# Optimization experiments

Measured on AMD Instinct MI355X. Metric: run time of the kernel, lower is better.

Reference implementation:

```python
import jax, jax.numpy as jnp
import numpy as np

NEG_INF = jnp.float32(-1e30)  # stand-in for -inf; relu(-inf) == relu(-1e30) == 0


def setup_inputs() -> dict:
    key = jax.random.key(0)
    ks = jax.random.split(key, 8)
    B, S, E = 4, 4096, 512
    query = jax.random.normal(ks[0], (B, S, E), dtype=jnp.float32)
    k_in = jax.random.normal(ks[1], (B, S, E), dtype=jnp.float32)
    v_in = jax.random.normal(ks[2], (B, S, E), dtype=jnp.float32)
    mask = jax.random.randint(ks[3], (B, S, S), 0, 2) > 0  # bool [B,S,S]
    scale = 1.0 / np.sqrt(E)
    W1 = jax.random.uniform(ks[4], (E, E), jnp.float32, -scale, scale)
    b1 = jax.random.uniform(ks[5], (E,), jnp.float32, -scale, scale)
    W2 = jax.random.uniform(ks[6], (E, E), jnp.float32, -scale, scale)
    b2 = jax.random.uniform(ks[7], (E,), jnp.float32, -scale, scale)
    return {"query": query, "key": k_in, "value": v_in, "mask": mask,
            "W1": W1, "b1": b1, "W2": W2, "b2": b2}


def reference(query, key, value, mask, W1, b1, W2, b2):
    # key projection: nn.Linear -> x @ W.T + b
    k = jnp.einsum('bse,fe->bsf', key, W1) + b1
    # raw dot-product correlation scores [B, S, S]
    scores = jnp.einsum('bqe,bke->bqk', query, k)
    # module forces mask[:, :, 0] = True, then fills ~mask with -inf
    m = mask.at[:, :, 0].set(True)
    scores = jnp.where(m, scores, NEG_INF)
    # ReLU instead of softmax (no normalization); dropout is identity in eval
    alpha = jax.nn.relu(scores)
    # value projection then AV matmul
    v = jnp.einsum('bse,fe->bsf', value, W2) + b2
    out = jnp.einsum('bqk,bke->bqe', alpha, v)
    return out
```

## Files before the change

kernel.cpp:

```cpp
#include <hip/hip_runtime.h>
#include <cstdint>


typedef __bf16 bf16x8 __attribute__((ext_vector_type(8)));
typedef float f32x4 __attribute__((ext_vector_type(4)));

__device__ __forceinline__ unsigned short f2bf(float f) {
  unsigned int u = __float_as_uint(f);
  u += 0x7fffu + ((u >> 16) & 1u);
  return (unsigned short)(u >> 16);
}

__device__ __forceinline__ void async_load16(const void* g, void* l) {
  __builtin_amdgcn_global_load_lds(
      (const __attribute__((address_space(1))) unsigned int*)(uintptr_t)g,
      (__attribute__((address_space(3))) unsigned int*)(unsigned int)(uintptr_t)l,
      16, 0, 0);
}

__global__ void __launch_bounds__(256)
prep(const float* __restrict__ q, const float* __restrict__ k,
     const float* __restrict__ v, const float* __restrict__ w1,
     const float* __restrict__ w2, const int* __restrict__ m,
     unsigned short* __restrict__ qb, unsigned short* __restrict__ kb,
     unsigned short* __restrict__ vb, unsigned short* __restrict__ w1b,
     unsigned short* __restrict__ w2b, unsigned int* __restrict__ bits) {
  const int b = blockIdx.x, tid = threadIdx.x;
  if (b < 24576) {
    const int which = b >> 13;
    const int idx = (b & 8191) * 256 + tid;
    const float* in = (which == 0) ? q : (which == 1) ? k : v;
    unsigned short* out = (which == 0) ? qb : (which == 1) ? kb : vb;
    float4 f = ((const float4*)in)[idx];
    ushort4 o;
    o.x = f2bf(f.x); o.y = f2bf(f.y); o.z = f2bf(f.z); o.w = f2bf(f.w);
    ((ushort4*)out)[idx] = o;
  } else if (b < 25088) {
    const int which = (b - 24576) >> 8;
    const int idx = ((b - 24576) & 255) * 256 + tid;
    const float* in = (which == 0) ? w1 : w2;
    unsigned short* out = (which == 0) ? w1b : w2b;
    float4 f = ((const float4*)in)[idx];
    ushort4 o;
    o.x = f2bf(f.x); o.y = f2bf(f.y); o.z = f2bf(f.z); o.w = f2bf(f.w);
    ((ushort4*)out)[idx] = o;
  } else {
    const int lane = tid & 63;
    const size_t wid = (size_t)(b - 25088) * 4 + (tid >> 6);
    const size_t base = wid * 256;
    unsigned long long bl[4];
#pragma unroll
    for (int c = 0; c < 4; ++c) {
      size_t e = base + (size_t)c * 64 + lane;
      int col = (int)(e & 4095);
      bl[c] = __ballot((m[e] != 0) || (col == 0));
    }
    if (lane < 8)
      bits[base / 32 + lane] = (unsigned int)(bl[lane >> 1] >> ((lane & 1) * 32));
  }
}

__global__ void __launch_bounds__(256)
proj(const unsigned short* __restrict__ Kb, const unsigned short* __restrict__ W1b,
     unsigned short* __restrict__ Kp, const float* __restrict__ b1,
     const unsigned short* __restrict__ W2b, const unsigned short* __restrict__ Vb,
     unsigned short* __restrict__ Vpt, const float* __restrict__ b2) {
  constexpr int K = 512;
  constexpr long long SE = 4096LL * 512;
  __shared__ unsigned short sA[2 * 128 * 32];
  __shared__ unsigned short sB[2 * 128 * 32];

  const int L = blockIdx.x;
  const unsigned short *Ab, *Bb;
  unsigned short* C;
  const float* bias;
  int tm0, tn0, N, epi;
  if (L < 512) {
    tn0 = (L & 3) * 128; tm0 = (L >> 2) * 128;
    Ab = Kb; Bb = W1b; C = Kp; bias = b1; N = 512; epi = 0;
  } else {
    const int t = L - 512;
    tn0 = (t & 31) * 128; tm0 = ((t >> 5) & 3) * 128;
    const int bz = t >> 7;
    Ab = W2b; Bb = Vb + (size_t)bz * SE; C = Vpt + (size_t)bz * SE;
    bias = b2; N = 4096; epi = 1;
  }

  const int tid = threadIdx.x;
  const int lane = tid & 63, wave = tid >> 6;
  const int ldrow = lane >> 2, lcol = (lane & 3) * 8;
  const int wm = (wave >> 1) * 64, wn = (wave & 1) * 64;
  const int lr = lane & 15, lq = lane >> 4;

  f32x4 acc[4][4] = {};

  for (int k0 = 0; k0 < K; k0 += 64) {
#pragma unroll
    for (int g = 0; g < 2; ++g)
#pragma unroll
      for (int l = 0; l < 2; ++l) {
        const int row = wave * 32 + l * 16;
        async_load16(Ab + (size_t)(tm0 + row + ldrow) * K + (k0 + g * 32 + lcol),
                     &sA[g * 4096 + row * 32]);
        async_load16(Bb + (size_t)(tn0 + row + ldrow) * K + (k0 + g * 32 + lcol),
                     &sB[g * 4096 + row * 32]);
      }
    __syncthreads();
#pragma unroll
    for (int g = 0; g < 2; ++g) {
      bf16x8 af[4], bfr[4];
#pragma unroll
      for (int t = 0; t < 4; ++t) {
        af[t]  = *(const bf16x8*)&sA[g * 4096 + (wm + t * 16 + lr) * 32 + lq * 8];
        bfr[t] = *(const bf16x8*)&sB[g * 4096 + (wn + t * 16 + lr) * 32 + lq * 8];
      }
#pragma unroll
      for (int mt = 0; mt < 4; ++mt)
#pragma unroll
        for (int nt = 0; nt < 4; ++nt)
          acc[mt][nt] = __builtin_amdgcn_mfma_f32_16x16x32_bf16(af[mt], bfr[nt],
                                                                acc[mt][nt], 0, 0, 0);
    }
    __syncthreads();
  }

#pragma unroll
  for (int mt = 0; mt < 4; ++mt)
#pragma unroll
    for (int r = 0; r < 4; ++r) {
      const int mm = tm0 + wm + mt * 16 + lq * 4 + r;
#pragma unroll
      for (int nt = 0; nt < 4; ++nt) {
        const int n = tn0 + wn + nt * 16 + lr;
        float v = acc[mt][nt][r];
        v += (epi == 0) ? bias[n] : bias[mm];
        C[(size_t)mm * N + n] = f2bf(v);
      }
    }
}

template <int EPI>
__global__ void __launch_bounds__(512, 2)
gemm256(const unsigned short* __restrict__ A, const unsigned short* __restrict__ B,
        void* __restrict__ Cout, const unsigned int* __restrict__ mbits,
        int M, int N, int K,
        long long strA, long long strB, long long strC, long long strM) {
  __shared__ unsigned short sA[2][256][64];
  __shared__ unsigned short sB[2][256][64];

  int lin = blockIdx.x;
  lin = (lin & 7) * ((int)gridDim.x >> 3) + (lin >> 3);
  const int tilesN = N >> 8;
  const int tilesM = M >> 8;
  const int bx = lin % tilesN;
  const int by = (lin / tilesN) % tilesM;
  const int bz = lin / (tilesN * tilesM);

  const int tn0 = bx << 8, tm0 = by << 8;
  const unsigned short* Ab = A + (size_t)bz * strA;
  const unsigned short* Bb = B + (size_t)bz * strB;

  const int tid  = threadIdx.x;
  const int lane = tid & 63;
  const int w    = tid >> 6;
  const int wr   = w >> 2;
  const int wc   = w & 3;
  const int lr   = lane & 15;
  const int lq   = lane >> 4;

  const int srow = tid >> 3;
  const int scol = (((tid & 7) ^ (srow & 7)) << 3);
  const int sdst = tid << 4;

#define STAGE64(bufbase, g, t0, k0, R0)                                      \
  async_load16((g) + (size_t)((t0) + (R0) + srow) * K + (k0) + scol,         \
               (char*)(bufbase) + ((R0) << 7) + sdst)

  const int sxor  = (lr & 7) << 4;
  const int k0off = (lq << 4) ^ sxor;
  const int k1off = (64 | (lq << 4)) ^ sxor;
  const int aRow  = (wr * 128 + lr) * 128;
  const int bRow  = (wc * 64 + lr) * 128;

#define LDA(d, mh, mt2, kk)                                                  \
  (*(const bf16x8*)((const char*)sA[d] + aRow + (mh) * 8192 + (mt2) * 2048 + \
                    k##kk##off))
#define LDB(d, nh, nt2, kk)                                                  \
  (*(const bf16x8*)((const char*)sB[d] + bRow + (nh) * 4096 + (nt2) * 2048 + \
                    k##kk##off))

  f32x4 acc[8][4] = {};
  bf16x8 afr[4][2];
  bf16x8 bfr[4][2];

#define RDA(d, mh)                                                           \
  _Pragma("unroll") for (int mt2 = 0; mt2 < 4; ++mt2) {                      \
    afr[mt2][0] = LDA(d, mh, mt2, 0);                                        \
    afr[mt2][1] = LDA(d, mh, mt2, 1);                                        \
  }
#define RDB(d, nh)                                                           \
  _Pragma("unroll") for (int nt2 = 0; nt2 < 2; ++nt2) {                      \
    bfr[(nh) * 2 + nt2][0] = LDB(d, nh, nt2, 0);                             \
    bfr[(nh) * 2 + nt2][1] = LDB(d, nh, nt2, 1);                             \
  }
#define MFMAQ(mh, nh)                                                        \
  __builtin_amdgcn_s_setprio(1);                                             \
  _Pragma("unroll") for (int mt2 = 0; mt2 < 4; ++mt2)                        \
  _Pragma("unroll") for (int nt2 = 0; nt2 < 2; ++nt2) {                      \
    acc[(mh) * 4 + mt2][(nh) * 2 + nt2] =                                    \
        __builtin_amdgcn_mfma_f32_16x16x32_bf16(                             \
            afr[mt2][0], bfr[(nh) * 2 + nt2][0],                             \
            acc[(mh) * 4 + mt2][(nh) * 2 + nt2], 0, 0, 0);                   \
    acc[(mh) * 4 + mt2][(nh) * 2 + nt2] =                                    \
        __builtin_amdgcn_mfma_f32_16x16x32_bf16(                             \
            afr[mt2][1], bfr[(nh) * 2 + nt2][1],                             \
            acc[(mh) * 4 + mt2][(nh) * 2 + nt2], 0, 0, 0);                   \
  }                                                                          \
  __builtin_amdgcn_s_setprio(0);
#define BAR __builtin_amdgcn_s_barrier()

  const int nIter = K >> 7;

  STAGE64(sB[0], Bb, tn0, 0, 0);   STAGE64(sB[0], Bb, tn0, 0, 64);
  STAGE64(sB[0], Bb, tn0, 0, 128); STAGE64(sB[0], Bb, tn0, 0, 192);
  STAGE64(sA[0], Ab, tm0, 0, 0);   STAGE64(sA[0], Ab, tm0, 0, 64);
  STAGE64(sA[0], Ab, tm0, 0, 128); STAGE64(sA[0], Ab, tm0, 0, 192);
  STAGE64(sB[1], Bb, tn0, 64, 0);  STAGE64(sB[1], Bb, tn0, 64, 64);
  STAGE64(sB[1], Bb, tn0, 64, 128);STAGE64(sB[1], Bb, tn0, 64, 192);
  asm volatile("s_waitcnt vmcnt(4)" ::: "memory");
  BAR;

  for (int j = 0; j < nIter; ++j) {
    const int kb = j << 7;
    const bool pf = (j + 1 < nIter);
    RDA(0, 0); RDB(0, 0);
    STAGE64(sA[1], Ab, tm0, kb + 64, 0);
    STAGE64(sA[1], Ab, tm0, kb + 64, 64);
    BAR; MFMAQ(0, 0); BAR;
    RDB(0, 1);
    STAGE64(sA[1], Ab, tm0, kb + 64, 128);
    STAGE64(sA[1], Ab, tm0, kb + 64, 192);
    BAR; MFMAQ(0, 1); BAR;
    RDA(0, 1);
    if (pf) { STAGE64(sB[0], Bb, tn0, kb + 128, 0);
              STAGE64(sB[0], Bb, tn0, kb + 128, 64); }
    BAR; MFMAQ(1, 1); BAR;
    if (pf) { STAGE64(sB[0], Bb, tn0, kb + 128, 128);
              STAGE64(sB[0], Bb, tn0, kb + 128, 192); }
    BAR; MFMAQ(1, 0);
    if (pf) asm volatile("s_waitcnt vmcnt(4)" ::: "memory");
    else    asm volatile("s_waitcnt vmcnt(0)" ::: "memory");
    BAR;
    RDA(1, 0); RDB(1, 0);
    if (pf) { STAGE64(sA[0], Ab, tm0, kb + 128, 0);
              STAGE64(sA[0], Ab, tm0, kb + 128, 64); }
    BAR; MFMAQ(0, 0); BAR;
    RDB(1, 1);
    if (pf) { STAGE64(sA[0], Ab, tm0, kb + 128, 128);
              STAGE64(sA[0], Ab, tm0, kb + 128, 192); }
    BAR; MFMAQ(0, 1); BAR;
    RDA(1, 1);
    if (pf) { STAGE64(sB[1], Bb, tn0, kb + 192, 0);
              STAGE64(sB[1], Bb, tn0, kb + 192, 64); }
    BAR; MFMAQ(1, 1); BAR;
    if (pf) { STAGE64(sB[1], Bb, tn0, kb + 192, 128);
              STAGE64(sB[1], Bb, tn0, kb + 192, 192); }
    BAR; MFMAQ(1, 0);
    asm volatile("s_waitcnt vmcnt(4)" ::: "memory");
    BAR;
  }

#pragma unroll
  for (int mt = 0; mt < 8; ++mt) {
#pragma unroll
    for (int r = 0; r < 4; ++r) {
      const int m = tm0 + wr * 128 + mt * 16 + lq * 4 + r;
      unsigned long long w64 = 0;
      if constexpr (EPI == 2) {
        w64 = *(const unsigned long long*)&mbits[(size_t)bz * strM +
                                                 (size_t)m * (N >> 5) +
                                                 ((tn0 + wc * 64) >> 5)];
      }
#pragma unroll
      for (int nt = 0; nt < 4; ++nt) {
        const int n = tn0 + wc * 64 + nt * 16 + lr;
        float v = acc[mt][nt][r];
        if constexpr (EPI == 2) {
          v = ((w64 >> (nt * 16 + lr)) & 1ull) ? fmaxf(v, 0.f) : 0.f;
          ((unsigned short*)Cout)[(size_t)bz * strC + (size_t)m * N + n] = f2bf(v);
        } else {
          ((float*)Cout)[(size_t)bz * strC + (size_t)m * N + n] = v;
        }
      }
    }
  }
#undef STAGE64
#undef LDA
#undef LDB
#undef RDA
#undef RDB
#undef MFMAQ
#undef BAR
}

__global__ void __launch_bounds__(512, 2)
outgemm(const unsigned short* __restrict__ A, const unsigned short* __restrict__ B,
        float* __restrict__ Cout, int M, int N, int K,
        long long strA, long long strB, long long strC) {
  __shared__ unsigned short sA[2][256][64];
  __shared__ unsigned short sB[2][128][64];

  int lin = blockIdx.x;
  lin = (lin & 7) * ((int)gridDim.x >> 3) + (lin >> 3);
  const int tilesN = N >> 7;
  const int tilesM = M >> 8;
  const int bx = lin % tilesN;
  const int by = (lin / tilesN) % tilesM;
  const int bz = lin / (tilesN * tilesM);

  const int tn0 = bx << 7, tm0 = by << 8;
  const unsigned short* Ab = A + (size_t)bz * strA;
  const unsigned short* Bb = B + (size_t)bz * strB;

  const int tid  = threadIdx.x;
  const int lane = tid & 63;
  const int w    = tid >> 6;
  const int wr   = w >> 2;
  const int wc   = w & 3;
  const int lr   = lane & 15;
  const int lq   = lane >> 4;

  const int srow = tid >> 3;
  const int scol = (((tid & 7) ^ (srow & 7)) << 3);
  const int sdst = tid << 4;

#define OST(bufbase, g, t0, k0, R0)                                          \
  async_load16((g) + (size_t)((t0) + (R0) + srow) * K + (k0) + scol,         \
               (char*)(bufbase) + ((R0) << 7) + sdst)

  const int sxor  = (lr & 7) << 4;
  const int k0off = (lq << 4) ^ sxor;
  const int k1off = (64 | (lq << 4)) ^ sxor;
  const int aRow  = (wr * 128 + lr) * 128;
  const int bRow  = (wc * 32 + lr) * 128;

#define OLDA(d, mh, mt2, kk)                                                 \
  (*(const bf16x8*)((const char*)sA[d] + aRow + (mh) * 8192 + (mt2) * 2048 + \
                    k##kk##off))
#define OLDB(d, nt, kk)                                                      \
  (*(const bf16x8*)((const char*)sB[d] + bRow + (nt) * 2048 + k##kk##off))

  f32x4 acc[8][2] = {};
  bf16x8 afr[4][2];
  bf16x8 bfr[2][2];

#define ORDA(d, mh)                                                          \
  _Pragma("unroll") for (int mt2 = 0; mt2 < 4; ++mt2) {                      \
    afr[mt2][0] = OLDA(d, mh, mt2, 0);                                       \
    afr[mt2][1] = OLDA(d, mh, mt2, 1);                                       \
  }
#define ORDB(d, nt)                                                          \
  { bfr[nt][0] = OLDB(d, nt, 0); bfr[nt][1] = OLDB(d, nt, 1); }
#define OMFMAQ(mh, nt)                                                       \
  __builtin_amdgcn_s_setprio(1);                                             \
  _Pragma("unroll") for (int mt2 = 0; mt2 < 4; ++mt2) {                      \
    acc[(mh) * 4 + mt2][nt] = __builtin_amdgcn_mfma_f32_16x16x32_bf16(       \
        afr[mt2][0], bfr[nt][0], acc[(mh) * 4 + mt2][nt], 0, 0, 0);          \
    acc[(mh) * 4 + mt2][nt] = __builtin_amdgcn_mfma_f32_16x16x32_bf16(       \
        afr[mt2][1], bfr[nt][1], acc[(mh) * 4 + mt2][nt], 0, 0, 0);          \
  }                                                                          \
  __builtin_amdgcn_s_setprio(0);
#define OBAR __builtin_amdgcn_s_barrier()

  const int nIter = K >> 7;

  OST(sB[0], Bb, tn0, 0, 0);   OST(sB[0], Bb, tn0, 0, 64);
  OST(sA[0], Ab, tm0, 0, 0);   OST(sA[0], Ab, tm0, 0, 64);
  OST(sA[0], Ab, tm0, 0, 128); OST(sA[0], Ab, tm0, 0, 192);
  OST(sB[1], Bb, tn0, 64, 0);  OST(sB[1], Bb, tn0, 64, 64);
  asm volatile("s_waitcnt vmcnt(2)" ::: "memory");
  OBAR;

  for (int j = 0; j < nIter; ++j) {
    const int kb = j << 7;
    const bool pf = (j + 1 < nIter);
    ORDA(0, 0); ORDB(0, 0);
    OST(sA[1], Ab, tm0, kb + 64, 0);
    OST(sA[1], Ab, tm0, kb + 64, 64);
    OBAR; OMFMAQ(0, 0); OBAR;
    ORDB(0, 1);
    OST(sA[1], Ab, tm0, kb + 64, 128);
    OST(sA[1], Ab, tm0, kb + 64, 192);
    OBAR; OMFMAQ(0, 1); OBAR;
    ORDA(0, 1);
    if (pf) OST(sB[0], Bb, tn0, kb + 128, 0);
    OBAR; OMFMAQ(1, 1); OBAR;
    if (pf) OST(sB[0], Bb, tn0, kb + 128, 64);
    OBAR; OMFMAQ(1, 0);
    if (pf) asm volatile("s_waitcnt vmcnt(2)" ::: "memory");
    else    asm volatile("s_waitcnt vmcnt(0)" ::: "memory");
    OBAR;
    ORDA(1, 0); ORDB(1, 0);
    if (pf) { OST(sA[0], Ab, tm0, kb + 128, 0);
              OST(sA[0], Ab, tm0, kb + 128, 64); }
    OBAR; OMFMAQ(0, 0); OBAR;
    ORDB(1, 1);
    if (pf) { OST(sA[0], Ab, tm0, kb + 128, 128);
              OST(sA[0], Ab, tm0, kb + 128, 192); }
    OBAR; OMFMAQ(0, 1); OBAR;
    ORDA(1, 1);
    if (pf) OST(sB[1], Bb, tn0, kb + 192, 0);
    OBAR; OMFMAQ(1, 1); OBAR;
    if (pf) OST(sB[1], Bb, tn0, kb + 192, 64);
    OBAR; OMFMAQ(1, 0);
    asm volatile("s_waitcnt vmcnt(2)" ::: "memory");
    OBAR;
  }

#pragma unroll
  for (int mt = 0; mt < 8; ++mt) {
#pragma unroll
    for (int r = 0; r < 4; ++r) {
      const int m = tm0 + wr * 128 + mt * 16 + lq * 4 + r;
#pragma unroll
      for (int nt = 0; nt < 2; ++nt) {
        const int n = tn0 + wc * 32 + nt * 16 + lr;
        Cout[(size_t)bz * strC + (size_t)m * N + n] = acc[mt][nt][r];
      }
    }
  }
#undef OST
#undef OLDA
#undef OLDB
#undef ORDA
#undef ORDB
#undef OMFMAQ
#undef OBAR
}

extern "C" void kernel_launch(void* const* d_in, const int* in_sizes, int n_in,
                              void* d_out, int out_size, void* d_ws, size_t ws_size,
                              hipStream_t stream) {
  const float* query = (const float*)d_in[0];
  const float* key   = (const float*)d_in[1];
  const float* value = (const float*)d_in[2];
  const int*   mask  = (const int*)d_in[3];
  const float* W1    = (const float*)d_in[4];
  const float* b1    = (const float*)d_in[5];
  const float* W2    = (const float*)d_in[6];
  const float* b2    = (const float*)d_in[7];
  float* out = (float*)d_out;

  constexpr int B = 4, S = 4096, E = 512;
  constexpr long long BSE = (long long)B * S * E;
  constexpr long long SE  = (long long)S * E;
  constexpr long long SS  = (long long)S * S;
  constexpr long long BSS = (long long)B * S * S;
  constexpr long long EE  = (long long)E * E;

  char* ws = (char*)d_ws;
  unsigned short* Qb   = (unsigned short*)ws;  ws += BSE * 2;
  unsigned short* Kb   = (unsigned short*)ws;  ws += BSE * 2;
  unsigned short* Vb   = (unsigned short*)ws;  ws += BSE * 2;
  unsigned short* W1b  = (unsigned short*)ws;  ws += EE * 2;
  unsigned short* W2b  = (unsigned short*)ws;  ws += EE * 2;
  unsigned short* Kp   = (unsigned short*)ws;  ws += BSE * 2;
  unsigned short* Vpt  = (unsigned short*)ws;  ws += BSE * 2;
  unsigned short* alph = (unsigned short*)ws;  ws += BSS * 2;
  unsigned int*   mbit = (unsigned int*)ws;    ws += BSS / 8;

  prep<<<dim3(24576 + 512 + 65536), 256, 0, stream>>>(
      query, key, value, W1, W2, mask, Qb, Kb, Vb, W1b, W2b, mbit);

  proj<<<dim3(1024), 256, 0, stream>>>(Kb, W1b, Kp, b1, W2b, Vb, Vpt, b2);

  gemm256<2><<<dim3((S / 256) * (S / 256) * B), 512, 0, stream>>>(
      Qb, Kp, alph, mbit, S, S, E, SE, SE, SS, SS / 32);

  outgemm<<<dim3((E / 128) * (S / 256) * B), 512, 0, stream>>>(
      alph, Vpt, out, S, E, S, SS, SE, SE);
}
```

Measured before the change: 631.0 us.

## Make alpha GEMM persistent across batches and merge outgemm MFMA phases

The alpha score GEMM now launches one block per (m,n) tile and loops over all four batches. The K-stage pipeline runs continuously across batch boundaries, and the masked-ReLU epilogue is written every 8 K-steps before the accumulators are reset. The intent is to cut the pipeline prologue and drain per tile and keep the loads flowing across batches, at the cost of a grid four times smaller (256 blocks), which may underfill the CUs. The output GEMM also merges its MFMA quarter-phases into halves with fewer barriers, and its loads are batched together.

Result: slower. 691.9 us (+9.6%).

```diff
diff --git a/kernel.cpp b/kernel.cpp
--- a/kernel.cpp
+++ b/kernel.cpp
@@ -139,26 +139,20 @@
     }
 }
 
-template <int EPI>
 __global__ void __launch_bounds__(512, 2)
-gemm256(const unsigned short* __restrict__ A, const unsigned short* __restrict__ B,
-        void* __restrict__ Cout, const unsigned int* __restrict__ mbits,
-        int M, int N, int K,
-        long long strA, long long strB, long long strC, long long strM) {
+alpha256(const unsigned short* __restrict__ A, const unsigned short* __restrict__ B,
+         unsigned short* __restrict__ Cw, const unsigned int* __restrict__ mbits,
+         int M, int N, int K,
+         long long strA, long long strB, long long strC, long long strM) {
   __shared__ unsigned short sA[2][256][64];
   __shared__ unsigned short sB[2][256][64];
 
   int lin = blockIdx.x;
   lin = (lin & 7) * ((int)gridDim.x >> 3) + (lin >> 3);
-  const int tilesN = N >> 8;
-  const int tilesM = M >> 8;
-  const int bx = lin % tilesN;
-  const int by = (lin / tilesN) % tilesM;
-  const int bz = lin / (tilesN * tilesM);
+  const int bx = lin & 15;
+  const int by = lin >> 4;
 
   const int tn0 = bx << 8, tm0 = by << 8;
-  const unsigned short* Ab = A + (size_t)bz * strA;
-  const unsigned short* Bb = B + (size_t)bz * strB;
 
   const int tid  = threadIdx.x;
   const int lane = tid & 63;
@@ -172,9 +166,20 @@
   const int scol = (((tid & 7) ^ (srow & 7)) << 3);
   const int sdst = tid << 4;
 
-#define STAGE64(bufbase, g, t0, k0, R0)                                      \
-  async_load16((g) + (size_t)((t0) + (R0) + srow) * K + (k0) + scol,         \
-               (char*)(bufbase) + ((R0) << 7) + sdst)
+#define STG_A(bufbase, gk, R0)                                               \
+  if ((gk) < 32) {                                                           \
+    const unsigned short* P_ = A + (size_t)((gk) >> 3) * strA;               \
+    async_load16(P_ + (size_t)(tm0 + (R0) + srow) * K + (((gk) & 7) << 6) +  \
+                     scol,                                                   \
+                 (char*)(bufbase) + ((R0) << 7) + sdst);                     \
+  }
+#define STG_B(bufbase, gk, R0)                                               \
+  if ((gk) < 32) {                                                           \
+    const unsigned short* P_ = B + (size_t)((gk) >> 3) * strB;               \
+    async_load16(P_ + (size_t)(tn0 + (R0) + srow) * K + (((gk) & 7) << 6) +  \
+                     scol,                                                   \
+                 (char*)(bufbase) + ((R0) << 7) + sdst);                     \
+  }
 
   const int sxor  = (lr & 7) << 4;
   const int k0off = (lq << 4) ^ sxor;
@@ -219,82 +224,74 @@
   __builtin_amdgcn_s_setprio(0);
 #define BAR __builtin_amdgcn_s_barrier()
 
-  const int nIter = K >> 7;
-
-  STAGE64(sB[0], Bb, tn0, 0, 0);   STAGE64(sB[0], Bb, tn0, 0, 64);
-  STAGE64(sB[0], Bb, tn0, 0, 128); STAGE64(sB[0], Bb, tn0, 0, 192);
-  STAGE64(sA[0], Ab, tm0, 0, 0);   STAGE64(sA[0], Ab, tm0, 0, 64);
-  STAGE64(sA[0], Ab, tm0, 0, 128); STAGE64(sA[0], Ab, tm0, 0, 192);
-  STAGE64(sB[1], Bb, tn0, 64, 0);  STAGE64(sB[1], Bb, tn0, 64, 64);
-  STAGE64(sB[1], Bb, tn0, 64, 128);STAGE64(sB[1], Bb, tn0, 64, 192);
+  STG_B(sB[0], 0, 0);   STG_B(sB[0], 0, 64);
+  STG_B(sB[0], 0, 128); STG_B(sB[0], 0, 192);
+  STG_A(sA[0], 0, 0);   STG_A(sA[0], 0, 64);
+  STG_A(sA[0], 0, 128); STG_A(sA[0], 0, 192);
+  STG_B(sB[1], 1, 0);   STG_B(sB[1], 1, 64);
+  STG_B(sB[1], 1, 128); STG_B(sB[1], 1, 192);
   asm volatile("s_waitcnt vmcnt(4)" ::: "memory");
   BAR;
 
-  for (int j = 0; j < nIter; ++j) {
-    const int kb = j << 7;
-    const bool pf = (j + 1 < nIter);
+  for (int s = 0; s < 16; ++s) {
+    const int gk0 = 2 * s, gk1 = gk0 + 1;
     RDA(0, 0); RDB(0, 0);
-    STAGE64(sA[1], Ab, tm0, kb + 64, 0);
-    STAGE64(sA[1], Ab, tm0, kb + 64, 64);
+    STG_A(sA[1], gk1, 0); STG_A(sA[1], gk1, 64);
     BAR; MFMAQ(0, 0); BAR;
     RDB(0, 1);
-    STAGE64(sA[1], Ab, tm0, kb + 64, 128);
-    STAGE64(sA[1], Ab, tm0, kb + 64, 192);
+    STG_A(sA[1], gk1, 128); STG_A(sA[1], gk1, 192);
     BAR; MFMAQ(0, 1); BAR;
     RDA(0, 1);
-    if (pf) { STAGE64(sB[0], Bb, tn0, kb + 128, 0);
-              STAGE64(sB[0], Bb, tn0, kb + 128, 64); }
+    STG_B(sB[0], gk0 + 2, 0); STG_B(sB[0], gk0 + 2, 64);
     BAR; MFMAQ(1, 1); BAR;
-    if (pf) { STAGE64(sB[0], Bb, tn0, kb + 128, 128);
-              STAGE64(sB[0], Bb, tn0, kb + 128, 192); }
+    STG_B(sB[0], gk0 + 2, 128); STG_B(sB[0], gk0 + 2, 192);
     BAR; MFMAQ(1, 0);
-    if (pf) asm volatile("s_waitcnt vmcnt(4)" ::: "memory");
-    else    asm volatile("s_waitcnt vmcnt(0)" ::: "memory");
+    if (gk0 + 2 < 32) asm volatile("s_waitcnt vmcnt(4)" ::: "memory");
+    else              asm volatile("s_waitcnt vmcnt(0)" ::: "memory");
     BAR;
     RDA(1, 0); RDB(1, 0);
-    if (pf) { STAGE64(sA[0], Ab, tm0, kb + 128, 0);
-              STAGE64(sA[0], Ab, tm0, kb + 128, 64); }
+    STG_A(sA[0], gk0 + 2, 0); STG_A(sA[0], gk0 + 2, 64);
     BAR; MFMAQ(0, 0); BAR;
     RDB(1, 1);
-    if (pf) { STAGE64(sA[0], Ab, tm0, kb + 128, 128);
-              STAGE64(sA[0], Ab, tm0, kb + 128, 192); }
+    STG_A(sA[0], gk0 + 2, 128); STG_A(sA[0], gk0 + 2, 192);
     BAR; MFMAQ(0, 1); BAR;
     RDA(1, 1);
-    if (pf) { STAGE64(sB[1], Bb, tn0, kb + 192, 0);
-              STAGE64(sB[1], Bb, tn0, kb + 192, 64); }
+    STG_B(sB[1], gk0 + 3, 0); STG_B(sB[1], gk0 + 3, 64);
     BAR; MFMAQ(1, 1); BAR;
-    if (pf) { STAGE64(sB[1], Bb, tn0, kb + 192, 128);
-              STAGE64(sB[1], Bb, tn0, kb + 192, 192); }
+    STG_B(sB[1], gk0 + 3, 128); STG_B(sB[1], gk0 + 3, 192);
     BAR; MFMAQ(1, 0);
     asm volatile("s_waitcnt vmcnt(4)" ::: "memory");
     BAR;
-  }
-
-#pragma unroll
-  for (int mt = 0; mt < 8; ++mt) {
-#pragma unroll
-    for (int r = 0; r < 4; ++r) {
-      const int m = tm0 + wr * 128 + mt * 16 + lq * 4 + r;
-      unsigned long long w64 = 0;
-      if constexpr (EPI == 2) {
-        w64 = *(const unsigned long long*)&mbits[(size_t)bz * strM +
+
+    if ((s & 3) == 3) {
+      const int tz = s >> 2;
+#pragma unroll
+      for (int mt = 0; mt < 8; ++mt) {
+#pragma unroll
+        for (int r = 0; r < 4; ++r) {
+          const int m = tm0 + wr * 128 + mt * 16 + lq * 4 + r;
+          unsigned long long w64 =
+              *(const unsigned long long*)&mbits[(size_t)tz * strM +
                                                  (size_t)m * (N >> 5) +
                                                  ((tn0 + wc * 64) >> 5)];
-      }
-#pragma unroll
-      for (int nt = 0; nt < 4; ++nt) {
-        const int n = tn0 + wc * 64 + nt * 16 + lr;
-        float v = acc[mt][nt][r];
-        if constexpr (EPI == 2) {
-          v = ((w64 >> (nt * 16 + lr)) & 1ull) ? fmaxf(v, 0.f) : 0.f;
-          ((unsigned short*)Cout)[(size_t)bz * strC + (size_t)m * N + n] = f2bf(v);
-        } else {
-          ((float*)Cout)[(size_t)bz * strC + (size_t)m * N + n] = v;
+#pragma unroll
+          for (int nt = 0; nt < 4; ++nt) {
+            const int n = tn0 + wc * 64 + nt * 16 + lr;
+            float v = acc[mt][nt][r];
+            v = ((w64 >> (nt * 16 + lr)) & 1ull) ? fmaxf(v, 0.f) : 0.f;
+            Cw[(size_t)tz * strC + (size_t)m * N + n] = f2bf(v);
+          }
         }
       }
+      const f32x4 z = {0.f, 0.f, 0.f, 0.f};
+#pragma unroll
+      for (int mt = 0; mt < 8; ++mt)
+#pragma unroll
+        for (int nt = 0; nt < 4; ++nt) acc[mt][nt] = z;
     }
   }
-#undef STAGE64
+#undef STG_A
+#undef STG_B
 #undef LDA
 #undef LDB
 #undef RDA
@@ -359,11 +356,13 @@
     afr[mt2][0] = OLDA(d, mh, mt2, 0);                                       \
     afr[mt2][1] = OLDA(d, mh, mt2, 1);                                       \
   }
-#define ORDB(d, nt)                                                          \
-  { bfr[nt][0] = OLDB(d, nt, 0); bfr[nt][1] = OLDB(d, nt, 1); }
-#define OMFMAQ(mh, nt)                                                       \
+#define ORDBB(d)                                                             \
+  { bfr[0][0] = OLDB(d, 0, 0); bfr[0][1] = OLDB(d, 0, 1);                    \
+    bfr[1][0] = OLDB(d, 1, 0); bfr[1][1] = OLDB(d, 1, 1); }
+#define OMFMA16(mh)                                                          \
   __builtin_amdgcn_s_setprio(1);                                             \
-  _Pragma("unroll") for (int mt2 = 0; mt2 < 4; ++mt2) {                      \
+  _Pragma("unroll") for (int mt2 = 0; mt2 < 4; ++mt2)                        \
+  _Pragma("unroll") for (int nt = 0; nt < 2; ++nt) {                         \
     acc[(mh) * 4 + mt2][nt] = __builtin_amdgcn_mfma_f32_16x16x32_bf16(       \
         afr[mt2][0], bfr[nt][0], acc[(mh) * 4 + mt2][nt], 0, 0, 0);          \
     acc[(mh) * 4 + mt2][nt] = __builtin_amdgcn_mfma_f32_16x16x32_bf16(       \
@@ -384,36 +383,29 @@
   for (int j = 0; j < nIter; ++j) {
     const int kb = j << 7;
     const bool pf = (j + 1 < nIter);
-    ORDA(0, 0); ORDB(0, 0);
-    OST(sA[1], Ab, tm0, kb + 64, 0);
-    OST(sA[1], Ab, tm0, kb + 64, 64);
-    OBAR; OMFMAQ(0, 0); OBAR;
-    ORDB(0, 1);
-    OST(sA[1], Ab, tm0, kb + 64, 128);
-    OST(sA[1], Ab, tm0, kb + 64, 192);
-    OBAR; OMFMAQ(0, 1); OBAR;
+    ORDA(0, 0); ORDBB(0);
+    OST(sA[1], Ab, tm0, kb + 64, 0);   OST(sA[1], Ab, tm0, kb + 64, 64);
+    OST(sA[1], Ab, tm0, kb + 64, 128); OST(sA[1], Ab, tm0, kb + 64, 192);
+    OBAR; OMFMA16(0); OBAR;
     ORDA(0, 1);
-    if (pf) OST(sB[0], Bb, tn0, kb + 128, 0);
-    OBAR; OMFMAQ(1, 1); OBAR;
-    if (pf) OST(sB[0], Bb, tn0, kb + 128, 64);
-    OBAR; OMFMAQ(1, 0);
+    if (pf) { OST(sB[0], Bb, tn0, kb + 128, 0);
+              OST(sB[0], Bb, tn0, kb + 128, 64); }
+    OBAR; OMFMA16(1);
     if (pf) asm volatile("s_waitcnt vmcnt(2)" ::: "memory");
     else    asm volatile("s_waitcnt vmcnt(0)" ::: "memory");
     OBAR;
-    ORDA(1, 0); ORDB(1, 0);
+    ORDA(1, 0); ORDBB(1);
     if (pf) { OST(sA[0], Ab, tm0, kb + 128, 0);
-              OST(sA[0], Ab, tm0, kb + 128, 64); }
-    OBAR; OMFMAQ(0, 0); OBAR;
-    ORDB(1, 1);
-    if (pf) { OST(sA[0], Ab, tm0, kb + 128, 128);
+              OST(sA[0], Ab, tm0, kb + 128, 64);
+              OST(sA[0], Ab, tm0, kb + 128, 128);
               OST(sA[0], Ab, tm0, kb + 128, 192); }
-    OBAR; OMFMAQ(0, 1); OBAR;
+    OBAR; OMFMA16(0); OBAR;
     ORDA(1, 1);
-    if (pf) OST(sB[1], Bb, tn0, kb + 192, 0);
-    OBAR; OMFMAQ(1, 1); OBAR;
-    if (pf) OST(sB[1], Bb, tn0, kb + 192, 64);
-    OBAR; OMFMAQ(1, 0);
-    asm volatile("s_waitcnt vmcnt(2)" ::: "memory");
+    if (pf) { OST(sB[1], Bb, tn0, kb + 192, 0);
+              OST(sB[1], Bb, tn0, kb + 192, 64); }
+    OBAR; OMFMA16(1);
+    if (pf) asm volatile("s_waitcnt vmcnt(2)" ::: "memory");
+    else    asm volatile("s_waitcnt vmcnt(0)" ::: "memory");
     OBAR;
   }
 
@@ -433,8 +425,8 @@
 #undef OLDA
 #undef OLDB
 #undef ORDA
-#undef ORDB
-#undef OMFMAQ
+#undef ORDBB
+#undef OMFMA16
 #undef OBAR
 }
 
@@ -474,7 +466,7 @@
 
   proj<<<dim3(1024), 256, 0, stream>>>(Kb, W1b, Kp, b1, W2b, Vb, Vpt, b2);
 
-  gemm256<2><<<dim3((S / 256) * (S / 256) * B), 512, 0, stream>>>(
+  alpha256<<<dim3((S / 256) * (S / 256)), 512, 0, stream>>>(
       Qb, Kp, alph, mbit, S, S, E, SE, SE, SS, SS / 32);
 
   outgemm<<<dim3((E / 128) * (S / 256) * B), 512, 0, stream>>>(
```

## Make alpha GEMM persistent over batch and retile output GEMM to 128x256

Applied to the files above, without the earlier changes.

The scores/alpha kernel now launches 256 blocks, one per 256x256 tile, and each block loops over the 4 batches, dropping the per-batch grid dimension and the template epilogue switch. The output GEMM swaps its tile shape from 256x128 to 128x256 (M by N), loading more of the V operand per block and less of alpha, with adjusted staging and wait counts. The intent is to cut launch or tail imbalance and improve operand reuse. The risk is that only 256 blocks may underfill the GPU and serialize the batch work inside each block.

Result: slower. 725.2 us (+14.9%).

```diff
diff --git a/kernel.cpp b/kernel.cpp
--- a/kernel.cpp
+++ b/kernel.cpp
@@ -139,26 +139,19 @@
     }
 }
 
-template <int EPI>
 __global__ void __launch_bounds__(512, 2)
-gemm256(const unsigned short* __restrict__ A, const unsigned short* __restrict__ B,
-        void* __restrict__ Cout, const unsigned int* __restrict__ mbits,
-        int M, int N, int K,
-        long long strA, long long strB, long long strC, long long strM) {
+alpha256p(const unsigned short* __restrict__ A, const unsigned short* __restrict__ B,
+          unsigned short* __restrict__ Cw, const unsigned int* __restrict__ mbits,
+          int M, int N, int K,
+          long long strA, long long strB, long long strC, long long strM) {
   __shared__ unsigned short sA[2][256][64];
   __shared__ unsigned short sB[2][256][64];
 
   int lin = blockIdx.x;
-  lin = (lin & 7) * ((int)gridDim.x >> 3) + (lin >> 3);
-  const int tilesN = N >> 8;
-  const int tilesM = M >> 8;
-  const int bx = lin % tilesN;
-  const int by = (lin / tilesN) % tilesM;
-  const int bz = lin / (tilesN * tilesM);
-
+  lin = (lin & 7) * 32 + (lin >> 3);
+  const int bx = lin & 15;
+  const int by = lin >> 4;
   const int tn0 = bx << 8, tm0 = by << 8;
-  const unsigned short* Ab = A + (size_t)bz * strA;
-  const unsigned short* Bb = B + (size_t)bz * strB;
 
   const int tid  = threadIdx.x;
   const int lane = tid & 63;
@@ -189,7 +182,6 @@
   (*(const bf16x8*)((const char*)sB[d] + bRow + (nh) * 4096 + (nt2) * 2048 + \
                     k##kk##off))
 
-  f32x4 acc[8][4] = {};
   bf16x8 afr[4][2];
   bf16x8 bfr[4][2];
 
@@ -221,75 +213,76 @@
 
   const int nIter = K >> 7;
 
-  STAGE64(sB[0], Bb, tn0, 0, 0);   STAGE64(sB[0], Bb, tn0, 0, 64);
-  STAGE64(sB[0], Bb, tn0, 0, 128); STAGE64(sB[0], Bb, tn0, 0, 192);
-  STAGE64(sA[0], Ab, tm0, 0, 0);   STAGE64(sA[0], Ab, tm0, 0, 64);
-  STAGE64(sA[0], Ab, tm0, 0, 128); STAGE64(sA[0], Ab, tm0, 0, 192);
-  STAGE64(sB[1], Bb, tn0, 64, 0);  STAGE64(sB[1], Bb, tn0, 64, 64);
-  STAGE64(sB[1], Bb, tn0, 64, 128);STAGE64(sB[1], Bb, tn0, 64, 192);
-  asm volatile("s_waitcnt vmcnt(4)" ::: "memory");
-  BAR;
-
-  for (int j = 0; j < nIter; ++j) {
-    const int kb = j << 7;
-    const bool pf = (j + 1 < nIter);
-    RDA(0, 0); RDB(0, 0);
-    STAGE64(sA[1], Ab, tm0, kb + 64, 0);
-    STAGE64(sA[1], Ab, tm0, kb + 64, 64);
-    BAR; MFMAQ(0, 0); BAR;
-    RDB(0, 1);
-    STAGE64(sA[1], Ab, tm0, kb + 64, 128);
-    STAGE64(sA[1], Ab, tm0, kb + 64, 192);
-    BAR; MFMAQ(0, 1); BAR;
-    RDA(0, 1);
-    if (pf) { STAGE64(sB[0], Bb, tn0, kb + 128, 0);
-              STAGE64(sB[0], Bb, tn0, kb + 128, 64); }
-    BAR; MFMAQ(1, 1); BAR;
-    if (pf) { STAGE64(sB[0], Bb, tn0, kb + 128, 128);
-              STAGE64(sB[0], Bb, tn0, kb + 128, 192); }
-    BAR; MFMAQ(1, 0);
-    if (pf) asm volatile("s_waitcnt vmcnt(4)" ::: "memory");
-    else    asm volatile("s_waitcnt vmcnt(0)" ::: "memory");
-    BAR;
-    RDA(1, 0); RDB(1, 0);
-    if (pf) { STAGE64(sA[0], Ab, tm0, kb + 128, 0);
-              STAGE64(sA[0], Ab, tm0, kb + 128, 64); }
-    BAR; MFMAQ(0, 0); BAR;
-    RDB(1, 1);
-    if (pf) { STAGE64(sA[0], Ab, tm0, kb + 128, 128);
-              STAGE64(sA[0], Ab, tm0, kb + 128, 192); }
-    BAR; MFMAQ(0, 1); BAR;
-    RDA(1, 1);
-    if (pf) { STAGE64(sB[1], Bb, tn0, kb + 192, 0);
-              STAGE64(sB[1], Bb, tn0, kb + 192, 64); }
-    BAR; MFMAQ(1, 1); BAR;
-    if (pf) { STAGE64(sB[1], Bb, tn0, kb + 192, 128);
-              STAGE64(sB[1], Bb, tn0, kb + 192, 192); }
-    BAR; MFMAQ(1, 0);
+  for (int vz = 0; vz < 4; ++vz) {
+    const unsigned short* Ab = A + (size_t)vz * strA;
+    const unsigned short* Bb = B + (size_t)vz * strB;
+
+    f32x4 acc[8][4] = {};
+
+    STAGE64(sB[0], Bb, tn0, 0, 0);   STAGE64(sB[0], Bb, tn0, 0, 64);
+    STAGE64(sB[0], Bb, tn0, 0, 128); STAGE64(sB[0], Bb, tn0, 0, 192);
+    STAGE64(sA[0], Ab, tm0, 0, 0);   STAGE64(sA[0], Ab, tm0, 0, 64);
+    STAGE64(sA[0], Ab, tm0, 0, 128); STAGE64(sA[0], Ab, tm0, 0, 192);
+    STAGE64(sB[1], Bb, tn0, 64, 0);  STAGE64(sB[1], Bb, tn0, 64, 64);
+    STAGE64(sB[1], Bb, tn0, 64, 128);STAGE64(sB[1], Bb, tn0, 64, 192);
     asm volatile("s_waitcnt vmcnt(4)" ::: "memory");
     BAR;
-  }
-
-#pragma unroll
-  for (int mt = 0; mt < 8; ++mt) {
-#pragma unroll
-    for (int r = 0; r < 4; ++r) {
-      const int m = tm0 + wr * 128 + mt * 16 + lq * 4 + r;
-      unsigned long long w64 = 0;
-      if constexpr (EPI == 2) {
-        w64 = *(const unsigned long long*)&mbits[(size_t)bz * strM +
-                                                 (size_t)m * (N >> 5) +
-                                                 ((tn0 + wc * 64) >> 5)];
-      }
-#pragma unroll
-      for (int nt = 0; nt < 4; ++nt) {
-        const int n = tn0 + wc * 64 + nt * 16 + lr;
-        float v = acc[mt][nt][r];
-        if constexpr (EPI == 2) {
+
+    for (int j = 0; j < nIter; ++j) {
+      const int kb = j << 7;
+      const bool pf = (j + 1 < nIter);
+      RDA(0, 0); RDB(0, 0);
+      STAGE64(sA[1], Ab, tm0, kb + 64, 0);
+      STAGE64(sA[1], Ab, tm0, kb + 64, 64);
+      BAR; MFMAQ(0, 0); BAR;
+      RDB(0, 1);
+      STAGE64(sA[1], Ab, tm0, kb + 64, 128);
+      STAGE64(sA[1], Ab, tm0, kb + 64, 192);
+      BAR; MFMAQ(0, 1); BAR;
+      RDA(0, 1);
+      if (pf) { STAGE64(sB[0], Bb, tn0, kb + 128, 0);
+                STAGE64(sB[0], Bb, tn0, kb + 128, 64); }
+      BAR; MFMAQ(1, 1); BAR;
+      if (pf) { STAGE64(sB[0], Bb, tn0, kb + 128, 128);
+                STAGE64(sB[0], Bb, tn0, kb + 128, 192); }
+      BAR; MFMAQ(1, 0);
+      if (pf) asm volatile("s_waitcnt vmcnt(4)" ::: "memory");
+      else    asm volatile("s_waitcnt vmcnt(0)" ::: "memory");
+      BAR;
+      RDA(1, 0); RDB(1, 0);
+      if (pf) { STAGE64(sA[0], Ab, tm0, kb + 128, 0);
+                STAGE64(sA[0], Ab, tm0, kb + 128, 64); }
+      BAR; MFMAQ(0, 0); BAR;
+      RDB(1, 1);
+      if (pf) { STAGE64(sA[0], Ab, tm0, kb + 128, 128);
+                STAGE64(sA[0], Ab, tm0, kb + 128, 192); }
+      BAR; MFMAQ(0, 1); BAR;
+      RDA(1, 1);
+      if (pf) { STAGE64(sB[1], Bb, tn0, kb + 192, 0);
+                STAGE64(sB[1], Bb, tn0, kb + 192, 64); }
+      BAR; MFMAQ(1, 1); BAR;
+      if (pf) { STAGE64(sB[1], Bb, tn0, kb + 192, 128);
+                STAGE64(sB[1], Bb, tn0, kb + 192, 192); }
+      BAR; MFMAQ(1, 0);
+      asm volatile("s_waitcnt vmcnt(4)" ::: "memory");
+      BAR;
+    }
+
+#pragma unroll
+    for (int mt = 0; mt < 8; ++mt) {
+#pragma unroll
+      for (int r = 0; r < 4; ++r) {
+        const int m = tm0 + wr * 128 + mt * 16 + lq * 4 + r;
+        unsigned long long w64 =
+            *(const unsigned long long*)&mbits[(size_t)vz * strM +
+                                               (size_t)m * (N >> 5) +
+                                               ((tn0 + wc * 64) >> 5)];
+#pragma unroll
+        for (int nt = 0; nt < 4; ++nt) {
+          const int n = tn0 + wc * 64 + nt * 16 + lr;
+          float v = acc[mt][nt][r];
           v = ((w64 >> (nt * 16 + lr)) & 1ull) ? fmaxf(v, 0.f) : 0.f;
-          ((unsigned short*)Cout)[(size_t)bz * strC + (size_t)m * N + n] = f2bf(v);
-        } else {
-          ((float*)Cout)[(size_t)bz * strC + (size_t)m * N + n] = v;
+          Cw[(size_t)vz * strC + (size_t)m * N + n] = f2bf(v);
         }
       }
     }
@@ -304,21 +297,21 @@
 }
 
 __global__ void __launch_bounds__(512, 2)
-outgemm(const unsigned short* __restrict__ A, const unsigned short* __restrict__ B,
-        float* __restrict__ Cout, int M, int N, int K,
-        long long strA, long long strB, long long strC) {
-  __shared__ unsigned short sA[2][256][64];
-  __shared__ unsigned short sB[2][128][64];
+outg(const unsigned short* __restrict__ A, const unsigned short* __restrict__ B,
+     float* __restrict__ Cout, int M, int N, int K,
+     long long strA, long long strB, long long strC) {
+  __shared__ unsigned short sA[2][128][64];
+  __shared__ unsigned short sB[2][256][64];
 
   int lin = blockIdx.x;
   lin = (lin & 7) * ((int)gridDim.x >> 3) + (lin >> 3);
-  const int tilesN = N >> 7;
-  const int tilesM = M >> 8;
+  const int tilesN = N >> 8;
+  const int tilesM = M >> 7;
   const int bx = lin % tilesN;
   const int by = (lin / tilesN) % tilesM;
   const int bz = lin / (tilesN * tilesM);
 
-  const int tn0 = bx << 7, tm0 = by << 8;
+  const int tn0 = bx << 8, tm0 = by << 7;
   const unsigned short* Ab = A + (size_t)bz * strA;
   const unsigned short* Bb = B + (size_t)bz * strB;
 
@@ -341,33 +334,42 @@
   const int sxor  = (lr & 7) << 4;
   const int k0off = (lq << 4) ^ sxor;
   const int k1off = (64 | (lq << 4)) ^ sxor;
-  const int aRow  = (wr * 128 + lr) * 128;
-  const int bRow  = (wc * 32 + lr) * 128;
+  const int aRow  = (wr * 64 + lr) * 128;
+  const int bRow  = (wc * 64 + lr) * 128;
 
 #define OLDA(d, mh, mt2, kk)                                                 \
-  (*(const bf16x8*)((const char*)sA[d] + aRow + (mh) * 8192 + (mt2) * 2048 + \
+  (*(const bf16x8*)((const char*)sA[d] + aRow + (mh) * 4096 + (mt2) * 2048 + \
                     k##kk##off))
-#define OLDB(d, nt, kk)                                                      \
-  (*(const bf16x8*)((const char*)sB[d] + bRow + (nt) * 2048 + k##kk##off))
-
-  f32x4 acc[8][2] = {};
-  bf16x8 afr[4][2];
-  bf16x8 bfr[2][2];
+#define OLDB(d, nh, nt2, kk)                                                 \
+  (*(const bf16x8*)((const char*)sB[d] + bRow + (nh) * 4096 + (nt2) * 2048 + \
+                    k##kk##off))
+
+  f32x4 acc[4][4] = {};
+  bf16x8 afr[2][2];
+  bf16x8 bfr[4][2];
 
 #define ORDA(d, mh)                                                          \
-  _Pragma("unroll") for (int mt2 = 0; mt2 < 4; ++mt2) {                      \
+  _Pragma("unroll") for (int mt2 = 0; mt2 < 2; ++mt2) {                      \
     afr[mt2][0] = OLDA(d, mh, mt2, 0);                                       \
     afr[mt2][1] = OLDA(d, mh, mt2, 1);                                       \
   }
-#define ORDB(d, nt)                                                          \
-  { bfr[nt][0] = OLDB(d, nt, 0); bfr[nt][1] = OLDB(d, nt, 1); }
-#define OMFMAQ(mh, nt)                                                       \
+#define ORDB(d, nh)                                                          \
+  _Pragma("unroll") for (int nt2 = 0; nt2 < 2; ++nt2) {                      \
+    bfr[(nh) * 2 + nt2][0] = OLDB(d, nh, nt2, 0);                            \
+    bfr[(nh) * 2 + nt2][1] = OLDB(d, nh, nt2, 1);                            \
+  }
+#define OMFMAQ(mh, nh)                                                       \
   __builtin_amdgcn_s_setprio(1);                                             \
-  _Pragma("unroll") for (int mt2 = 0; mt2 < 4; ++mt2) {                      \
-    acc[(mh) * 4 + mt2][nt] = __builtin_amdgcn_mfma_f32_16x16x32_bf16(       \
-        afr[mt2][0], bfr[nt][0], acc[(mh) * 4 + mt2][nt], 0, 0, 0);          \
-    acc[(mh) * 4 + mt2][nt] = __builtin_amdgcn_mfma_f32_16x16x32_bf16(       \
-        afr[mt2][1], bfr[nt][1], acc[(mh) * 4 + mt2][nt], 0, 0, 0);          \
+  _Pragma("unroll") for (int mt2 = 0; mt2 < 2; ++mt2)                        \
+  _Pragma("unroll") for (int nt2 = 0; nt2 < 2; ++nt2) {                      \
+    acc[(mh) * 2 + mt2][(nh) * 2 + nt2] =                                    \
+        __builtin_amdgcn_mfma_f32_16x16x32_bf16(                             \
+            afr[mt2][0], bfr[(nh) * 2 + nt2][0],                             \
+            acc[(mh) * 2 + mt2][(nh) * 2 + nt2], 0, 0, 0);                   \
+    acc[(mh) * 2 + mt2][(nh) * 2 + nt2] =                                    \
+        __builtin_amdgcn_mfma_f32_16x16x32_bf16(                             \
+            afr[mt2][1], bfr[(nh) * 2 + nt2][1],                             \
+            acc[(mh) * 2 + mt2][(nh) * 2 + nt2], 0, 0, 0);                   \
   }                                                                          \
   __builtin_amdgcn_s_setprio(0);
 #define OBAR __builtin_amdgcn_s_barrier()
@@ -375,10 +377,11 @@
   const int nIter = K >> 7;
 
   OST(sB[0], Bb, tn0, 0, 0);   OST(sB[0], Bb, tn0, 0, 64);
+  OST(sB[0], Bb, tn0, 0, 128); OST(sB[0], Bb, tn0, 0, 192);
   OST(sA[0], Ab, tm0, 0, 0);   OST(sA[0], Ab, tm0, 0, 64);
-  OST(sA[0], Ab, tm0, 0, 128); OST(sA[0], Ab, tm0, 0, 192);
   OST(sB[1], Bb, tn0, 64, 0);  OST(sB[1], Bb, tn0, 64, 64);
-  asm volatile("s_waitcnt vmcnt(2)" ::: "memory");
+  OST(sB[1], Bb, tn0, 64, 128);OST(sB[1], Bb, tn0, 64, 192);
+  asm volatile("s_waitcnt vmcnt(4)" ::: "memory");
   OBAR;
 
   for (int j = 0; j < nIter; ++j) {
@@ -389,15 +392,15 @@
     OST(sA[1], Ab, tm0, kb + 64, 64);
     OBAR; OMFMAQ(0, 0); OBAR;
     ORDB(0, 1);
-    OST(sA[1], Ab, tm0, kb + 64, 128);
-    OST(sA[1], Ab, tm0, kb + 64, 192);
     OBAR; OMFMAQ(0, 1); OBAR;
     ORDA(0, 1);
-    if (pf) OST(sB[0], Bb, tn0, kb + 128, 0);
+    if (pf) { OST(sB[0], Bb, tn0, kb + 128, 0);
+              OST(sB[0], Bb, tn0, kb + 128, 64); }
     OBAR; OMFMAQ(1, 1); OBAR;
-    if (pf) OST(sB[0], Bb, tn0, kb + 128, 64);
+    if (pf) { OST(sB[0], Bb, tn0, kb + 128, 128);
+              OST(sB[0], Bb, tn0, kb + 128, 192); }
     OBAR; OMFMAQ(1, 0);
-    if (pf) asm volatile("s_waitcnt vmcnt(2)" ::: "memory");
+    if (pf) asm volatile("s_waitcnt vmcnt(4)" ::: "memory");
     else    asm volatile("s_waitcnt vmcnt(0)" ::: "memory");
     OBAR;
     ORDA(1, 0); ORDB(1, 0);
@@ -405,27 +408,27 @@
               OST(sA[0], Ab, tm0, kb + 128, 64); }
     OBAR; OMFMAQ(0, 0); OBAR;
     ORDB(1, 1);
-    if (pf) { OST(sA[0], Ab, tm0, kb + 128, 128);
-              OST(sA[0], Ab, tm0, kb + 128, 192); }
     OBAR; OMFMAQ(0, 1); OBAR;
     ORDA(1, 1);
-    if (pf) OST(sB[1], Bb, tn0, kb + 192, 0);
+    if (pf) { OST(sB[1], Bb, tn0, kb + 192, 0);
+              OST(sB[1], Bb, tn0, kb + 192, 64); }
     OBAR; OMFMAQ(1, 1); OBAR;
-    if (pf) OST(sB[1], Bb, tn0, kb + 192, 64);
+    if (pf) { OST(sB[1], Bb, tn0, kb + 192, 128);
+              OST(sB[1], Bb, tn0, kb + 192, 192); }
     OBAR; OMFMAQ(1, 0);
-    asm volatile("s_waitcnt vmcnt(2)" ::: "memory");
+    asm volatile("s_waitcnt vmcnt(4)" ::: "memory");
     OBAR;
   }
 
 #pragma unroll
-  for (int mt = 0; mt < 8; ++mt) {
+  for (int mi = 0; mi < 4; ++mi) {
 #pragma unroll
     for (int r = 0; r < 4; ++r) {
-      const int m = tm0 + wr * 128 + mt * 16 + lq * 4 + r;
-#pragma unroll
-      for (int nt = 0; nt < 2; ++nt) {
-        const int n = tn0 + wc * 32 + nt * 16 + lr;
-        Cout[(size_t)bz * strC + (size_t)m * N + n] = acc[mt][nt][r];
+      const int m = tm0 + wr * 64 + mi * 16 + lq * 4 + r;
+#pragma unroll
+      for (int ni = 0; ni < 4; ++ni) {
+        const int n = tn0 + wc * 64 + ni * 16 + lr;
+        Cout[(size_t)bz * strC + (size_t)m * N + n] = acc[mi][ni][r];
       }
     }
   }
@@ -474,9 +477,9 @@
 
   proj<<<dim3(1024), 256, 0, stream>>>(Kb, W1b, Kp, b1, W2b, Vb, Vpt, b2);
 
-  gemm256<2><<<dim3((S / 256) * (S / 256) * B), 512, 0, stream>>>(
+  alpha256p<<<dim3((S / 256) * (S / 256)), 512, 0, stream>>>(
       Qb, Kp, alph, mbit, S, S, E, SE, SE, SS, SS / 32);
 
-  outgemm<<<dim3((E / 128) * (S / 256) * B), 512, 0, stream>>>(
+  outg<<<dim3((E / 256) * (S / 128) * B), 512, 0, stream>>>(
       alph, Vpt, out, S, E, S, SS, SE, SE);
 }
```
